# Optimization experiments

Hardware: AMD Instinct MI355X
Metric: run time of the kernel (lower is better)

Reference implementation:

```python
import jax, jax.numpy as jnp
import numpy as np

N_USER = 100000
N_ITEM = 100000
N_EDGE = 1600000
IN_U = 128
IN_I = 128
OUT = 64
NEG_SLOPE = 0.01  # torch F.leaky_relu default


def setup_inputs() -> dict:
    key = jax.random.key(0)
    ks = jax.random.split(key, 12)
    return {
        'feat_user': jax.random.normal(ks[0], (N_USER, IN_U), jnp.float32),
        'feat_item': jax.random.normal(ks[1], (N_ITEM, IN_I), jnp.float32),
        'W_user': jax.random.normal(ks[2], (IN_U, OUT), jnp.float32) * 0.05,
        'b_user': jax.random.normal(ks[3], (OUT,), jnp.float32) * 0.05,
        'W_item': jax.random.normal(ks[4], (IN_I, OUT), jnp.float32) * 0.05,
        'b_item': jax.random.normal(ks[5], (OUT,), jnp.float32) * 0.05,
        'attn_w': jax.random.normal(ks[6], (2 * OUT, 1), jnp.float32) * 0.05,
        'src_u2i': jax.random.randint(ks[7], (N_EDGE,), 0, N_USER),
        'dst_u2i': jax.random.randint(ks[8], (N_EDGE,), 0, N_ITEM),
        'src_i2u': jax.random.randint(ks[9], (N_EDGE,), 0, N_ITEM),
        'dst_i2u': jax.random.randint(ks[10], (N_EDGE,), 0, N_USER),
    }


def _segment_softmax(e, seg, num_segments):
    # e: [E], seg: [E] destination ids -> softmax over edges sharing a dst
    m = jax.ops.segment_max(e, seg, num_segments=num_segments)
    ex = jnp.exp(e - m[seg])
    s = jax.ops.segment_sum(ex, seg, num_segments=num_segments)
    return ex / s[seg]


def _etype_aggregate(Wh_src, Wh_dst, attn_w, src, dst, n_dst):
    # gather per-edge src/dst projected features: [E, OUT]
    zs = Wh_src[src]
    zd = Wh_dst[dst]
    # attn([zs || zd]) == zs @ a_src + zd @ a_dst (split the 2*OUT weight)
    a_src, a_dst = attn_w[:OUT, 0], attn_w[OUT:, 0]
    e = zs @ a_src + zd @ a_dst  # [E]
    e = jnp.where(e > 0, e, NEG_SLOPE * e)  # leaky_relu
    alpha = _segment_softmax(e, dst, n_dst)  # [E]
    # weighted scatter-sum into destination nodes
    return jax.ops.segment_sum(alpha[:, None] * zs, dst, num_segments=n_dst)


def reference(feat_user, feat_item, W_user, b_user, W_item, b_item, attn_w,
              src_u2i, dst_u2i, src_i2u, dst_i2u):
    Wh_user = feat_user @ W_user + b_user  # fc['user'] (etype 'user': user->item)
    Wh_item = feat_item @ W_item + b_item  # fc['item'] (etype 'item': item->user)
    # etype 'user': user -> item; dst attention feature is Wh_item on item nodes
    h_item = _etype_aggregate(Wh_user, Wh_item, attn_w, src_u2i, dst_u2i, N_ITEM)
    # etype 'item': item -> user
    h_user = _etype_aggregate(Wh_item, Wh_user, attn_w, src_i2u, dst_i2u, N_USER)
    # update_nodes sums all 'self_*' per ntype; each ntype has exactly one here
    return jnp.concatenate([h_user, h_item], axis=0)  # [N_USER+N_ITEM, OUT]
```

## Files before the change

### kernel.cpp

```cpp
#include <hip/hip_runtime.h>
#include <hip/hip_bf16.h>

#define NU 100000
#define NI 100000
#define NE 1600000
#define KIN 128
#define KOUT 64

#define NCOPY 8
#define PBK 128
#define NP 782
#define CAP2 384
#define CHUNK 4096
#define SRTSZ (NCOPY * CAP2 + PBK * 7)
#define AGG_THREADS 512
#define NWAVE 8

#define LIN_ROWS 64
#define LIN_GRID 512
#define LIN_ITERS 1563

typedef short bf16x8 __attribute__((ext_vector_type(8)));
typedef float f32x4  __attribute__((ext_vector_type(4)));

__device__ __forceinline__ unsigned short f2bf(float f) {
    unsigned u = __float_as_uint(f);
    unsigned r = (u + 0x7fffu + ((u >> 16) & 1u)) >> 16;
    return (unsigned short)r;
}
__device__ __forceinline__ float bf2f(unsigned short h) {
    return __uint_as_float(((unsigned)h) << 16);
}
__device__ __forceinline__ void split_bf16(float f, unsigned short& h, unsigned short& l) {
    h = f2bf(f);
    float r = f - bf2f(h);
    l = f2bf(r);
}

__global__ __launch_bounds__(256) void linear_attn_kernel(
    const float* __restrict__ A0, const float* __restrict__ W0, const float* __restrict__ bv0,
    const float* __restrict__ A1, const float* __restrict__ W1, const float* __restrict__ bv1,
    const float* __restrict__ attn,
    unsigned short* __restrict__ Wh0, float* __restrict__ su0, float* __restrict__ sd0,
    unsigned short* __restrict__ Wh1, float* __restrict__ su1, float* __restrict__ sd1)
{
    __shared__ float Al[LIN_ROWS * 132];
    __shared__ __align__(16) unsigned short Wph[4 * 4 * 64 * 8];
    __shared__ __align__(16) unsigned short Wpl[4 * 4 * 64 * 8];

    int half = gridDim.x >> 1;
    bool second = blockIdx.x >= (unsigned)half;
    const float* A = second ? A1 : A0;
    const float* W = second ? W1 : W0;
    const float* bvec = second ? bv1 : bv0;
    unsigned short* Wh = second ? Wh1 : Wh0;
    float* s_src = second ? su1 : su0;
    float* s_dst = second ? sd1 : sd0;
    int blk = second ? (blockIdx.x - half) : blockIdx.x;

    int t = threadIdx.x;
    int l   = t & 63;
    int wv  = t >> 6;
    int ln  = l & 15;
    int grp = l >> 4;

    for (int i = 0; i < 4; i++) {
        int s = t + 256 * i;
        int sl = s & 63, nt = (s >> 6) & 3, ks = s >> 8;
        int kb = ks * 32 + (sl >> 4) * 8;
        int n  = nt * 16 + (sl & 15);
        unsigned short h8[8], l8[8];
        #pragma unroll
        for (int j = 0; j < 8; j++) {
            float w = W[(size_t)(kb + j) * KOUT + n];
            split_bf16(w, h8[j], l8[j]);
        }
        int base = ((ks * 4 + nt) * 64 + sl) * 8;
        #pragma unroll
        for (int j = 0; j < 8; j++) { Wph[base + j] = h8[j]; Wpl[base + j] = l8[j]; }
    }

    float asl[4], adl[4], bl4[4];
    #pragma unroll
    for (int nt = 0; nt < 4; nt++) {
        asl[nt] = attn[nt * 16 + ln];
        adl[nt] = attn[64 + nt * 16 + ln];
        bl4[nt] = bvec[nt * 16 + ln];
    }

    int arow = wv * 16 + ln;

    for (int c = blk; c < LIN_ITERS; c += half) {
        int rowbase = c * LIN_ROWS;
        __syncthreads();
        for (int g = t; g < LIN_ROWS * 32; g += 256) {
            int rr = g >> 5;
            int q  = g & 31;
            float4 v = {0.f, 0.f, 0.f, 0.f};
            int grow = rowbase + rr;
            if (grow < NU) v = ((const float4*)(A + (size_t)grow * 128))[q];
            *(float4*)&Al[rr * 132 + q * 4] = v;
        }
        __syncthreads();

        f32x4 acc0 = {bl4[0], bl4[0], bl4[0], bl4[0]};
        f32x4 acc1 = {bl4[1], bl4[1], bl4[1], bl4[1]};
        f32x4 acc2 = {bl4[2], bl4[2], bl4[2], bl4[2]};
        f32x4 acc3 = {bl4[3], bl4[3], bl4[3], bl4[3]};

        #pragma unroll
        for (int ks = 0; ks < 4; ks++) {
            int k0 = ks * 32 + grp * 8;
            const float* ap = &Al[arow * 132 + k0];
            float4 va = *(const float4*)ap;
            float4 vb = *(const float4*)(ap + 4);
            float av[8] = {va.x, va.y, va.z, va.w, vb.x, vb.y, vb.z, vb.w};
            bf16x8 ahi, alo;
            #pragma unroll
            for (int j = 0; j < 8; j++) {
                unsigned short h, lo2;
                split_bf16(av[j], h, lo2);
                ahi[j] = (short)h; alo[j] = (short)lo2;
            }
            #pragma unroll
            for (int nt = 0; nt < 4; nt++) {
                bf16x8 bhi = *(const bf16x8*)&Wph[((ks * 4 + nt) * 64 + l) * 8];
                bf16x8 blo = *(const bf16x8*)&Wpl[((ks * 4 + nt) * 64 + l) * 8];
                f32x4 a = (nt == 0) ? acc0 : (nt == 1) ? acc1 : (nt == 2) ? acc2 : acc3;
                a = __builtin_amdgcn_mfma_f32_16x16x32_bf16(ahi, bhi, a, 0, 0, 0);
                a = __builtin_amdgcn_mfma_f32_16x16x32_bf16(ahi, blo, a, 0, 0, 0);
                a = __builtin_amdgcn_mfma_f32_16x16x32_bf16(alo, bhi, a, 0, 0, 0);
                if (nt == 0) acc0 = a; else if (nt == 1) acc1 = a; else if (nt == 2) acc2 = a; else acc3 = a;
            }
        }

        int growbase = rowbase + wv * 16;
        f32x4 accs[4] = {acc0, acc1, acc2, acc3};
        #pragma unroll
        for (int nt = 0; nt < 4; nt++) {
            #pragma unroll
            for (int r = 0; r < 4; r++) {
                int row = growbase + grp * 4 + r;
                if (row < NU) Wh[(size_t)row * KOUT + nt * 16 + ln] = f2bf(accs[nt][r]);
            }
        }
        #pragma unroll
        for (int r = 0; r < 4; r++) {
            float p1 = accs[0][r] * asl[0] + accs[1][r] * asl[1] + accs[2][r] * asl[2] + accs[3][r] * asl[3];
            float p2 = accs[0][r] * adl[0] + accs[1][r] * adl[1] + accs[2][r] * adl[2] + accs[3][r] * adl[3];
            #pragma unroll
            for (int off = 1; off < 16; off <<= 1) {
                p1 += __shfl_xor(p1, off);
                p2 += __shfl_xor(p2, off);
            }
            int row = growbase + grp * 4 + r;
            if (ln == 0 && row < NU) { s_src[row] = p1; s_dst[row] = p2; }
        }
    }
}

__global__ __launch_bounds__(256) void scatter_kernel(
    const int* __restrict__ src_u2i, const int* __restrict__ dst_u2i,
    const int* __restrict__ src_i2u, const int* __restrict__ dst_i2u,
    int* __restrict__ cur_item, int* __restrict__ cur_user,
    int* __restrict__ ebuf_item, int* __restrict__ ebuf_user,
    int nE, int nbs)
{
    __shared__ int raw[CHUNK];
    __shared__ unsigned short bkt[CHUNK];
    __shared__ int srt_[CHUNK];
    __shared__ unsigned short sbk[CHUNK];
    __shared__ int cnt[NP];
    __shared__ int gb[NP];
    __shared__ int pb[NP];
    __shared__ int lc[NP];

    bool u2i = blockIdx.x < (unsigned)nbs;
    int blk = u2i ? blockIdx.x : (blockIdx.x - nbs);
    int copy = blockIdx.x & (NCOPY - 1);
    const int* src = u2i ? src_u2i : src_i2u;
    const int* dst = u2i ? dst_u2i : dst_i2u;
    int* cur  = (u2i ? cur_item : cur_user) + copy * NP;
    int* ebuf = (u2i ? ebuf_item : ebuf_user) + (size_t)copy * NP * CAP2;

    int t = threadIdx.x;
    for (int i = t; i < NP; i += 256) cnt[i] = 0;
    __syncthreads();

    int e0 = blk * CHUNK;
    int n = nE - e0; if (n > CHUNK) n = CHUNK;

    for (int j = t; j < n; j += 256) {
        int s = src[e0 + j], d = dst[e0 + j];
        int b = d >> 7;
        raw[j] = s | ((d & 127) << 17);
        bkt[j] = (unsigned short)b;
        atomicAdd(&cnt[b], 1);
    }
    __syncthreads();

    for (int b = t; b < NP; b += 256) {
        int c = cnt[b];
        gb[b] = c ? atomicAdd(&cur[b], c) : 0;
    }
    if (t < 64) {
        int lo = t * 13;
        int hi = lo + 13; if (hi > NP) hi = NP; if (lo > NP) lo = NP;
        int s = 0;
        for (int i = lo; i < hi; i++) s += cnt[i];
        int run = s;
        #pragma unroll
        for (int off = 1; off < 64; off <<= 1) {
            int v = __shfl_up(run, off);
            if (t >= off) run += v;
        }
        int excl = run - s;
        for (int i = lo; i < hi; i++) {
            pb[i] = excl; lc[i] = excl;
            excl += cnt[i];
        }
    }
    __syncthreads();

    for (int j = t; j < n; j += 256) {
        int b = bkt[j];
        int p = atomicAdd(&lc[b], 1);
        srt_[p] = raw[j];
        sbk[p] = (unsigned short)b;
    }
    __syncthreads();

    for (int j = t; j < n; j += 256) {
        int b = sbk[j];
        int pos = gb[b] + (j - pb[b]);
        if (pos < CAP2) ebuf[(size_t)b * CAP2 + pos] = srt_[j];
    }
}

__global__ __launch_bounds__(AGG_THREADS) void agg_kernel(
    const int* __restrict__ cur_item, const int* __restrict__ cur_user,
    const int* __restrict__ ebuf_item, const int* __restrict__ ebuf_user,
    const float* __restrict__ su_user, const float* __restrict__ sd_item,
    const float* __restrict__ su_item, const float* __restrict__ sd_user,
    const unsigned short* __restrict__ Wh_user, const unsigned short* __restrict__ Wh_item,
    float* __restrict__ h_item, float* __restrict__ h_user)
{
    __shared__ int   raw[SRTSZ];
    __shared__ int   srt[SRTSZ];
    __shared__ int   offs[NCOPY + 1];
    __shared__ int   cnt[PBK];
    __shared__ int   base[PBK + 1];
    __shared__ int   cursor[PBK];
    __shared__ float sdl[PBK];

    int bid = blockIdx.x;
    bool item_side = bid < NP;
    int b = item_side ? bid : bid - NP;
    const int*   cur  = item_side ? cur_item : cur_user;
    const int*   ebuf = item_side ? ebuf_item : ebuf_user;
    const float* ssrc = item_side ? su_user : su_item;
    const float* sdst = item_side ? sd_item : sd_user;
    const unsigned short* Whs = item_side ? Wh_user : Wh_item;
    float* h = item_side ? h_item : h_user;

    int t = threadIdx.x;
    if (t < PBK) {
        cnt[t] = 0;
        int node = b * PBK + t;
        sdl[t] = (node < NU) ? sdst[node] : 0.f;
    }
    if (t == 0) {
        int a = 0;
        #pragma unroll
        for (int c = 0; c < NCOPY; c++) {
            offs[c] = a;
            int cc = cur[c * NP + b];
            if (cc > CAP2) cc = CAP2;
            a += cc;
        }
        offs[NCOPY] = a;
    }
    for (int j = t; j < SRTSZ; j += AGG_THREADS) srt[j] = 0;
    __syncthreads();

    int total = offs[NCOPY];

    for (int j = t; j < total; j += AGG_THREADS) {
        int c = 0;
        while (j >= offs[c + 1]) c++;
        int e = ebuf[((size_t)c * NP + b) * CAP2 + (j - offs[c])];
        raw[j] = e;
        atomicAdd(&cnt[e >> 17], 1);
    }
    __syncthreads();

    if (t == 0) {
        int a = 0;
        for (int i = 0; i < PBK; i++) {
            base[i] = a; cursor[i] = a;
            a += (cnt[i] + 7) & ~7;
        }
        base[PBK] = a;
    }
    __syncthreads();

    for (int j = t; j < total; j += AGG_THREADS) {
        int e = raw[j];
        int p = atomicAdd(&cursor[e >> 17], 1);
        srt[p] = e;
    }
    __syncthreads();

    int lane = t & 63;
    int wv = t >> 6;

    float* wgt = (float*)raw;
    for (int dl = wv; dl < PBK; dl += NWAVE) {
        int jb = base[dl], cc = cnt[dl], pc = base[dl + 1] - jb;
        float sd = sdl[dl];
        for (int k = lane; k < pc; k += 64) {
            float w = 0.f;
            if (k < cc) {
                int s = srt[jb + k] & 0x1FFFF;
                float ev = ssrc[s] + sd;
                ev = ev > 0.f ? ev : 0.01f * ev;
                w = __expf(ev);
            }
            wgt[jb + k] = w;
        }
    }
    __syncthreads();

    int sub = lane >> 4;
    int ch4 = (lane & 15) << 2;
    const unsigned short* WhCh = Whs + ch4;
    for (int dl = wv; dl < PBK; dl += NWAVE) {
        int node = b * PBK + dl;
        if (node >= NU) break;
        int jb = base[dl];
        int pc = base[dl + 1] - jb;
        int cc = cnt[dl];
        float ax = 0.f, ay = 0.f, az = 0.f, aw = 0.f, ssum = 0.f;
        for (int q = 0; q < pc; q += 8) {
            int j0 = jb + q + sub;
            int j1 = j0 + 4;
            int e0 = srt[j0];
            int e1 = srt[j1];
            float w0 = wgt[j0];
            float w1 = wgt[j1];
            uint2 u0 = *(const uint2*)(WhCh + ((size_t)(e0 & 0x1FFFF) << 6));
            uint2 u1 = *(const uint2*)(WhCh + ((size_t)(e1 & 0x1FFFF) << 6));
            ax += w0 * __uint_as_float(u0.x << 16)        + w1 * __uint_as_float(u1.x << 16);
            ay += w0 * __uint_as_float(u0.x & 0xffff0000u)+ w1 * __uint_as_float(u1.x & 0xffff0000u);
            az += w0 * __uint_as_float(u0.y << 16)        + w1 * __uint_as_float(u1.y << 16);
            aw += w0 * __uint_as_float(u0.y & 0xffff0000u)+ w1 * __uint_as_float(u1.y & 0xffff0000u);
            ssum += w0 + w1;
        }
        #pragma unroll
        for (int off = 16; off <= 32; off <<= 1) {
            ax += __shfl_xor(ax, off);
            ay += __shfl_xor(ay, off);
            az += __shfl_xor(az, off);
            aw += __shfl_xor(aw, off);
            ssum += __shfl_xor(ssum, off);
        }
        if (sub == 0) {
            float inv = (cc > 0) ? 1.f / ssum : 0.f;
            float4 o = {ax * inv, ay * inv, az * inv, aw * inv};
            *(float4*)(h + (size_t)node * KOUT + ch4) = o;
        }
    }
}

extern "C" void kernel_launch(void* const* d_in, const int* in_sizes, int n_in,
                              void* d_out, int out_size, void* d_ws, size_t ws_size,
                              hipStream_t stream)
{
    const float* feat_user = (const float*)d_in[0];
    const float* feat_item = (const float*)d_in[1];
    const float* W_user    = (const float*)d_in[2];
    const float* b_user    = (const float*)d_in[3];
    const float* W_item    = (const float*)d_in[4];
    const float* b_item    = (const float*)d_in[5];
    const float* attn_w    = (const float*)d_in[6];
    const int*   src_u2i   = (const int*)d_in[7];
    const int*   dst_u2i   = (const int*)d_in[8];
    const int*   src_i2u   = (const int*)d_in[9];
    const int*   dst_i2u   = (const int*)d_in[10];

    float* out    = (float*)d_out;
    float* h_user = out;
    float* h_item = out + (size_t)NU * KOUT;

    char* p = (char*)d_ws;
    unsigned short* Wh_user = (unsigned short*)p; p += (size_t)NU * KOUT * 2;
    unsigned short* Wh_item = (unsigned short*)p; p += (size_t)NI * KOUT * 2;
    float* su_user = (float*)p; p += NU * 4;
    float* sd_user = (float*)p; p += NU * 4;
    float* su_item = (float*)p; p += NI * 4;
    float* sd_item = (float*)p; p += NI * 4;
    int* cur_item  = (int*)p; p += (size_t)NCOPY * NP * 4;
    int* cur_user  = (int*)p; p += (size_t)NCOPY * NP * 4;
    int* ebuf_item = (int*)p; p += (size_t)NCOPY * NP * CAP2 * 4;
    int* ebuf_user = (int*)p; p += (size_t)NCOPY * NP * CAP2 * 4;

    hipMemsetAsync(cur_item, 0, (size_t)2 * NCOPY * NP * 4, stream);

    int nbs = (NE + CHUNK - 1) / CHUNK;
    scatter_kernel<<<2 * nbs, 256, 0, stream>>>(src_u2i, dst_u2i, src_i2u, dst_i2u,
                                                cur_item, cur_user, ebuf_item, ebuf_user,
                                                NE, nbs);
    linear_attn_kernel<<<LIN_GRID, 256, 0, stream>>>(feat_user, W_user, b_user,
                                                     feat_item, W_item, b_item, attn_w,
                                                     Wh_user, su_user, sd_user,
                                                     Wh_item, su_item, sd_item);
    agg_kernel<<<2 * NP, AGG_THREADS, 0, stream>>>(cur_item, cur_user, ebuf_item, ebuf_user,
                                                   su_user, sd_item, su_item, sd_user,
                                                   Wh_user, Wh_item, h_item, h_user);
}
```

Measured before the change: 317.9 us.

## Merge scatter and linear kernels into one interleaved launch; widen agg gathers

The edge-bucketing scatter kernel and the MFMA linear/attention kernel become one launch, with block IDs interleaved so memory-bound scatter blocks and compute-bound GEMM blocks can share the GPU at the same time and one launch boundary disappears. The agg kernel replaces a serial single-thread prefix over 128 buckets with a wave-level shuffle scan. Its gather now reads 16-byte vectors of 8 bf16 channels per lane, with 8 lanes per row and 16 edges per step, plus a tail step. The merged kernel uses a 65KB shared buffer sized for the larger role, which may lower occupancy for scatter blocks.

```diff
diff --git a/kernel.cpp b/kernel.cpp
--- a/kernel.cpp
+++ b/kernel.cpp
@@ -36,204 +36,211 @@
     float r = f - bf2f(h);
     l = f2bf(r);
 }
-
-__global__ __launch_bounds__(256) void linear_attn_kernel(
+__device__ __forceinline__ float blo(unsigned u) { return __uint_as_float(u << 16); }
+__device__ __forceinline__ float bhi(unsigned u) { return __uint_as_float(u & 0xffff0000u); }
+
+__global__ __launch_bounds__(256) void prep_kernel(
+    const int* __restrict__ src_u2i, const int* __restrict__ dst_u2i,
+    const int* __restrict__ src_i2u, const int* __restrict__ dst_i2u,
+    int* __restrict__ cur_item, int* __restrict__ cur_user,
+    int* __restrict__ ebuf_item, int* __restrict__ ebuf_user, int nE, int nbs,
     const float* __restrict__ A0, const float* __restrict__ W0, const float* __restrict__ bv0,
     const float* __restrict__ A1, const float* __restrict__ W1, const float* __restrict__ bv1,
     const float* __restrict__ attn,
     unsigned short* __restrict__ Wh0, float* __restrict__ su0, float* __restrict__ sd0,
     unsigned short* __restrict__ Wh1, float* __restrict__ su1, float* __restrict__ sd1)
 {
-    __shared__ float Al[LIN_ROWS * 132];
-    __shared__ __align__(16) unsigned short Wph[4 * 4 * 64 * 8];
-    __shared__ __align__(16) unsigned short Wpl[4 * 4 * 64 * 8];
-
-    int half = gridDim.x >> 1;
-    bool second = blockIdx.x >= (unsigned)half;
-    const float* A = second ? A1 : A0;
-    const float* W = second ? W1 : W0;
-    const float* bvec = second ? bv1 : bv0;
-    unsigned short* Wh = second ? Wh1 : Wh0;
-    float* s_src = second ? su1 : su0;
-    float* s_dst = second ? sd1 : sd0;
-    int blk = second ? (blockIdx.x - half) : blockIdx.x;
+    __shared__ __align__(16) char smem[66560];
+
+    int bid = blockIdx.x;
+    int nsc = 2 * nbs;
+    int ninter = (nsc < LIN_GRID ? nsc : LIN_GRID) * 2;
+    bool is_lin; int sid;
+    if (bid < ninter) { is_lin = (bid & 1); sid = bid >> 1; }
+    else { is_lin = false; sid = ninter / 2 + (bid - ninter); }
 
     int t = threadIdx.x;
-    int l   = t & 63;
-    int wv  = t >> 6;
-    int ln  = l & 15;
-    int grp = l >> 4;
-
-    for (int i = 0; i < 4; i++) {
-        int s = t + 256 * i;
-        int sl = s & 63, nt = (s >> 6) & 3, ks = s >> 8;
-        int kb = ks * 32 + (sl >> 4) * 8;
-        int n  = nt * 16 + (sl & 15);
-        unsigned short h8[8], l8[8];
-        #pragma unroll
-        for (int j = 0; j < 8; j++) {
-            float w = W[(size_t)(kb + j) * KOUT + n];
-            split_bf16(w, h8[j], l8[j]);
-        }
-        int base = ((ks * 4 + nt) * 64 + sl) * 8;
-        #pragma unroll
-        for (int j = 0; j < 8; j++) { Wph[base + j] = h8[j]; Wpl[base + j] = l8[j]; }
-    }
-
-    float asl[4], adl[4], bl4[4];
-    #pragma unroll
-    for (int nt = 0; nt < 4; nt++) {
-        asl[nt] = attn[nt * 16 + ln];
-        adl[nt] = attn[64 + nt * 16 + ln];
-        bl4[nt] = bvec[nt * 16 + ln];
-    }
-
-    int arow = wv * 16 + ln;
-
-    for (int c = blk; c < LIN_ITERS; c += half) {
-        int rowbase = c * LIN_ROWS;
+
+    if (!is_lin) {
+        int* raw  = (int*)smem;
+        unsigned short* bkt = (unsigned short*)(smem + 16384);
+        int* srt_ = (int*)(smem + 24576);
+        unsigned short* sbk = (unsigned short*)(smem + 40960);
+        int* cnt = (int*)(smem + 49152);
+        int* gb  = (int*)(smem + 49152 + 4 * NP);
+        int* pb  = (int*)(smem + 49152 + 8 * NP);
+        int* lc  = (int*)(smem + 49152 + 12 * NP);
+
+        bool u2i = sid < nbs;
+        int blk = u2i ? sid : (sid - nbs);
+        int copy = sid & (NCOPY - 1);
+        const int* src = u2i ? src_u2i : src_i2u;
+        const int* dst = u2i ? dst_u2i : dst_i2u;
+        int* cur  = (u2i ? cur_item : cur_user) + copy * NP;
+        int* ebuf = (u2i ? ebuf_item : ebuf_user) + (size_t)copy * NP * CAP2;
+
+        for (int i = t; i < NP; i += 256) cnt[i] = 0;
         __syncthreads();
-        for (int g = t; g < LIN_ROWS * 32; g += 256) {
-            int rr = g >> 5;
-            int q  = g & 31;
-            float4 v = {0.f, 0.f, 0.f, 0.f};
-            int grow = rowbase + rr;
-            if (grow < NU) v = ((const float4*)(A + (size_t)grow * 128))[q];
-            *(float4*)&Al[rr * 132 + q * 4] = v;
+
+        int e0 = blk * CHUNK;
+        int n = nE - e0; if (n > CHUNK) n = CHUNK;
+
+        for (int j = t; j < n; j += 256) {
+            int s = src[e0 + j], d = dst[e0 + j];
+            int b = d >> 7;
+            raw[j] = s | ((d & 127) << 17);
+            bkt[j] = (unsigned short)b;
+            atomicAdd(&cnt[b], 1);
         }
         __syncthreads();
 
-        f32x4 acc0 = {bl4[0], bl4[0], bl4[0], bl4[0]};
-        f32x4 acc1 = {bl4[1], bl4[1], bl4[1], bl4[1]};
-        f32x4 acc2 = {bl4[2], bl4[2], bl4[2], bl4[2]};
-        f32x4 acc3 = {bl4[3], bl4[3], bl4[3], bl4[3]};
-
-        #pragma unroll
-        for (int ks = 0; ks < 4; ks++) {
-            int k0 = ks * 32 + grp * 8;
-            const float* ap = &Al[arow * 132 + k0];
-            float4 va = *(const float4*)ap;
-            float4 vb = *(const float4*)(ap + 4);
-            float av[8] = {va.x, va.y, va.z, va.w, vb.x, vb.y, vb.z, vb.w};
-            bf16x8 ahi, alo;
+        for (int b = t; b < NP; b += 256) {
+            int c = cnt[b];
+            gb[b] = c ? atomicAdd(&cur[b], c) : 0;
+        }
+        if (t < 64) {
+            int lo = t * 13;
+            int hi = lo + 13; if (hi > NP) hi = NP; if (lo > NP) lo = NP;
+            int s = 0;
+            for (int i = lo; i < hi; i++) s += cnt[i];
+            int run = s;
+            #pragma unroll
+            for (int off = 1; off < 64; off <<= 1) {
+                int v = __shfl_up(run, off);
+                if (t >= off) run += v;
+            }
+            int excl = run - s;
+            for (int i = lo; i < hi; i++) {
+                pb[i] = excl; lc[i] = excl;
+                excl += cnt[i];
+            }
+        }
+        __syncthreads();
+
+        for (int j = t; j < n; j += 256) {
+            int b = bkt[j];
+            int p = atomicAdd(&lc[b], 1);
+            srt_[p] = raw[j];
+            sbk[p] = (unsigned short)b;
+        }
+        __syncthreads();
+
+        for (int j = t; j < n; j += 256) {
+            int b = sbk[j];
+            int pos = gb[b] + (j - pb[b]);
+            if (pos < CAP2) ebuf[(size_t)b * CAP2 + pos] = srt_[j];
+        }
+    } else {
+        float* Al = (float*)smem;
+        unsigned short* Wph = (unsigned short*)(smem + 33792);
+        unsigned short* Wpl = (unsigned short*)(smem + 50176);
+
+        int half = LIN_GRID / 2;
+        bool second = sid >= half;
+        const float* A = second ? A1 : A0;
+        const float* W = second ? W1 : W0;
+        const float* bvec = second ? bv1 : bv0;
+        unsigned short* Wh = second ? Wh1 : Wh0;
+        float* s_src = second ? su1 : su0;
+        float* s_dst = second ? sd1 : sd0;
+        int blk = second ? (sid - half) : sid;
+
+        int l   = t & 63;
+        int wv  = t >> 6;
+        int ln  = l & 15;
+        int grp = l >> 4;
+
+        for (int i = 0; i < 4; i++) {
+            int s = t + 256 * i;
+            int sl = s & 63, nt = (s >> 6) & 3, ks = s >> 8;
+            int kb = ks * 32 + (sl >> 4) * 8;
+            int nn = nt * 16 + (sl & 15);
+            int base = ((ks * 4 + nt) * 64 + sl) * 8;
             #pragma unroll
             for (int j = 0; j < 8; j++) {
                 unsigned short h, lo2;
-                split_bf16(av[j], h, lo2);
-                ahi[j] = (short)h; alo[j] = (short)lo2;
-            }
-            #pragma unroll
-            for (int nt = 0; nt < 4; nt++) {
-                bf16x8 bhi = *(const bf16x8*)&Wph[((ks * 4 + nt) * 64 + l) * 8];
-                bf16x8 blo = *(const bf16x8*)&Wpl[((ks * 4 + nt) * 64 + l) * 8];
-                f32x4 a = (nt == 0) ? acc0 : (nt == 1) ? acc1 : (nt == 2) ? acc2 : acc3;
-                a = __builtin_amdgcn_mfma_f32_16x16x32_bf16(ahi, bhi, a, 0, 0, 0);
-                a = __builtin_amdgcn_mfma_f32_16x16x32_bf16(ahi, blo, a, 0, 0, 0);
-                a = __builtin_amdgcn_mfma_f32_16x16x32_bf16(alo, bhi, a, 0, 0, 0);
-                if (nt == 0) acc0 = a; else if (nt == 1) acc1 = a; else if (nt == 2) acc2 = a; else acc3 = a;
-            }
-        }
-
-        int growbase = rowbase + wv * 16;
-        f32x4 accs[4] = {acc0, acc1, acc2, acc3};
+                split_bf16(W[(size_t)(kb + j) * KOUT + nn], h, lo2);
+                Wph[base + j] = h; Wpl[base + j] = lo2;
+            }
+        }
+
+        float asl[4], adl[4], bl4[4];
         #pragma unroll
         for (int nt = 0; nt < 4; nt++) {
+            asl[nt] = attn[nt * 16 + ln];
+            adl[nt] = attn[64 + nt * 16 + ln];
+            bl4[nt] = bvec[nt * 16 + ln];
+        }
+
+        int arow = wv * 16 + ln;
+
+        for (int c = blk; c < LIN_ITERS; c += half) {
+            int rowbase = c * LIN_ROWS;
+            __syncthreads();
+            for (int g = t; g < LIN_ROWS * 32; g += 256) {
+                int rr = g >> 5;
+                int q  = g & 31;
+                float4 v = {0.f, 0.f, 0.f, 0.f};
+                int grow = rowbase + rr;
+                if (grow < NU) v = ((const float4*)(A + (size_t)grow * 128))[q];
+                *(float4*)&Al[rr * 132 + q * 4] = v;
+            }
+            __syncthreads();
+
+            f32x4 acc0 = {bl4[0], bl4[0], bl4[0], bl4[0]};
+            f32x4 acc1 = {bl4[1], bl4[1], bl4[1], bl4[1]};
+            f32x4 acc2 = {bl4[2], bl4[2], bl4[2], bl4[2]};
+            f32x4 acc3 = {bl4[3], bl4[3], bl4[3], bl4[3]};
+
+            #pragma unroll
+            for (int ks = 0; ks < 4; ks++) {
+                int k0 = ks * 32 + grp * 8;
+                const float* ap = &Al[arow * 132 + k0];
+                float4 va = *(const float4*)ap;
+                float4 vb = *(const float4*)(ap + 4);
+                float av[8] = {va.x, va.y, va.z, va.w, vb.x, vb.y, vb.z, vb.w};
+                bf16x8 ahi, alo;
+                #pragma unroll
+                for (int j = 0; j < 8; j++) {
+                    unsigned short h, lo2;
+                    split_bf16(av[j], h, lo2);
+                    ahi[j] = (short)h; alo[j] = (short)lo2;
+                }
+                #pragma unroll
+                for (int nt = 0; nt < 4; nt++) {
+                    bf16x8 bhi8 = *(const bf16x8*)&Wph[((ks * 4 + nt) * 64 + l) * 8];
+                    bf16x8 blo8 = *(const bf16x8*)&Wpl[((ks * 4 + nt) * 64 + l) * 8];
+                    f32x4 a = (nt == 0) ? acc0 : (nt == 1) ? acc1 : (nt == 2) ? acc2 : acc3;
+                    a = __builtin_amdgcn_mfma_f32_16x16x32_bf16(ahi, bhi8, a, 0, 0, 0);
+                    a = __builtin_amdgcn_mfma_f32_16x16x32_bf16(ahi, blo8, a, 0, 0, 0);
+                    a = __builtin_amdgcn_mfma_f32_16x16x32_bf16(alo, bhi8, a, 0, 0, 0);
+                    if (nt == 0) acc0 = a; else if (nt == 1) acc1 = a; else if (nt == 2) acc2 = a; else acc3 = a;
+                }
+            }
+
+            int growbase = rowbase + wv * 16;
+            f32x4 accs[4] = {acc0, acc1, acc2, acc3};
+            #pragma unroll
+            for (int nt = 0; nt < 4; nt++) {
+                #pragma unroll
+                for (int r = 0; r < 4; r++) {
+                    int row = growbase + grp * 4 + r;
+                    if (row < NU) Wh[(size_t)row * KOUT + nt * 16 + ln] = f2bf(accs[nt][r]);
+                }
+            }
             #pragma unroll
             for (int r = 0; r < 4; r++) {
+                float p1 = accs[0][r] * asl[0] + accs[1][r] * asl[1] + accs[2][r] * asl[2] + accs[3][r] * asl[3];
+                float p2 = accs[0][r] * adl[0] + accs[1][r] * adl[1] + accs[2][r] * adl[2] + accs[3][r] * adl[3];
+                #pragma unroll
+                for (int off = 1; off < 16; off <<= 1) {
+                    p1 += __shfl_xor(p1, off);
+                    p2 += __shfl_xor(p2, off);
+                }
                 int row = growbase + grp * 4 + r;
-                if (row < NU) Wh[(size_t)row * KOUT + nt * 16 + ln] = f2bf(accs[nt][r]);
-            }
-        }
-        #pragma unroll
-        for (int r = 0; r < 4; r++) {
-            float p1 = accs[0][r] * asl[0] + accs[1][r] * asl[1] + accs[2][r] * asl[2] + accs[3][r] * asl[3];
-            float p2 = accs[0][r] * adl[0] + accs[1][r] * adl[1] + accs[2][r] * adl[2] + accs[3][r] * adl[3];
-            #pragma unroll
-            for (int off = 1; off < 16; off <<= 1) {
-                p1 += __shfl_xor(p1, off);
-                p2 += __shfl_xor(p2, off);
-            }
-            int row = growbase + grp * 4 + r;
-            if (ln == 0 && row < NU) { s_src[row] = p1; s_dst[row] = p2; }
-        }
-    }
-}
-
-__global__ __launch_bounds__(256) void scatter_kernel(
-    const int* __restrict__ src_u2i, const int* __restrict__ dst_u2i,
-    const int* __restrict__ src_i2u, const int* __restrict__ dst_i2u,
-    int* __restrict__ cur_item, int* __restrict__ cur_user,
-    int* __restrict__ ebuf_item, int* __restrict__ ebuf_user,
-    int nE, int nbs)
-{
-    __shared__ int raw[CHUNK];
-    __shared__ unsigned short bkt[CHUNK];
-    __shared__ int srt_[CHUNK];
-    __shared__ unsigned short sbk[CHUNK];
-    __shared__ int cnt[NP];
-    __shared__ int gb[NP];
-    __shared__ int pb[NP];
-    __shared__ int lc[NP];
-
-    bool u2i = blockIdx.x < (unsigned)nbs;
-    int blk = u2i ? blockIdx.x : (blockIdx.x - nbs);
-    int copy = blockIdx.x & (NCOPY - 1);
-    const int* src = u2i ? src_u2i : src_i2u;
-    const int* dst = u2i ? dst_u2i : dst_i2u;
-    int* cur  = (u2i ? cur_item : cur_user) + copy * NP;
-    int* ebuf = (u2i ? ebuf_item : ebuf_user) + (size_t)copy * NP * CAP2;
-
-    int t = threadIdx.x;
-    for (int i = t; i < NP; i += 256) cnt[i] = 0;
-    __syncthreads();
-
-    int e0 = blk * CHUNK;
-    int n = nE - e0; if (n > CHUNK) n = CHUNK;
-
-    for (int j = t; j < n; j += 256) {
-        int s = src[e0 + j], d = dst[e0 + j];
-        int b = d >> 7;
-        raw[j] = s | ((d & 127) << 17);
-        bkt[j] = (unsigned short)b;
-        atomicAdd(&cnt[b], 1);
-    }
-    __syncthreads();
-
-    for (int b = t; b < NP; b += 256) {
-        int c = cnt[b];
-        gb[b] = c ? atomicAdd(&cur[b], c) : 0;
-    }
-    if (t < 64) {
-        int lo = t * 13;
-        int hi = lo + 13; if (hi > NP) hi = NP; if (lo > NP) lo = NP;
-        int s = 0;
-        for (int i = lo; i < hi; i++) s += cnt[i];
-        int run = s;
-        #pragma unroll
-        for (int off = 1; off < 64; off <<= 1) {
-            int v = __shfl_up(run, off);
-            if (t >= off) run += v;
-        }
-        int excl = run - s;
-        for (int i = lo; i < hi; i++) {
-            pb[i] = excl; lc[i] = excl;
-            excl += cnt[i];
-        }
-    }
-    __syncthreads();
-
-    for (int j = t; j < n; j += 256) {
-        int b = bkt[j];
-        int p = atomicAdd(&lc[b], 1);
-        srt_[p] = raw[j];
-        sbk[p] = (unsigned short)b;
-    }
-    __syncthreads();
-
-    for (int j = t; j < n; j += 256) {
-        int b = sbk[j];
-        int pos = gb[b] + (j - pb[b]);
-        if (pos < CAP2) ebuf[(size_t)b * CAP2 + pos] = srt_[j];
+                if (ln == 0 && row < NU) { s_src[row] = p1; s_dst[row] = p2; }
+            }
+        }
     }
 }
 
@@ -294,13 +301,21 @@
     }
     __syncthreads();
 
-    if (t == 0) {
-        int a = 0;
-        for (int i = 0; i < PBK; i++) {
-            base[i] = a; cursor[i] = a;
-            a += (cnt[i] + 7) & ~7;
-        }
-        base[PBK] = a;
+    if (t < 64) {
+        int i0 = 2 * t, i1 = 2 * t + 1;
+        int c0 = (cnt[i0] + 7) & ~7;
+        int c1 = (cnt[i1] + 7) & ~7;
+        int s = c0 + c1;
+        int run = s;
+        #pragma unroll
+        for (int off = 1; off < 64; off <<= 1) {
+            int v = __shfl_up(run, off);
+            if (t >= off) run += v;
+        }
+        int excl = run - s;
+        base[i0] = excl;      cursor[i0] = excl;
+        base[i1] = excl + c0; cursor[i1] = excl + c0;
+        if (t == 63) base[PBK] = run;
     }
     __syncthreads();
 
@@ -331,43 +346,60 @@
     }
     __syncthreads();
 
-    int sub = lane >> 4;
-    int ch4 = (lane & 15) << 2;
-    const unsigned short* WhCh = Whs + ch4;
+    int sub = lane >> 3;
+    int ch8 = (lane & 7) << 3;
+    const unsigned short* WhCh = Whs + ch8;
     for (int dl = wv; dl < PBK; dl += NWAVE) {
         int node = b * PBK + dl;
         if (node >= NU) break;
         int jb = base[dl];
         int pc = base[dl + 1] - jb;
         int cc = cnt[dl];
-        float ax = 0.f, ay = 0.f, az = 0.f, aw = 0.f, ssum = 0.f;
-        for (int q = 0; q < pc; q += 8) {
+        float acc[8] = {0.f, 0.f, 0.f, 0.f, 0.f, 0.f, 0.f, 0.f};
+        float ssum = 0.f;
+        int q = 0;
+        for (; q + 16 <= pc; q += 16) {
             int j0 = jb + q + sub;
-            int j1 = j0 + 4;
-            int e0 = srt[j0];
-            int e1 = srt[j1];
-            float w0 = wgt[j0];
-            float w1 = wgt[j1];
-            uint2 u0 = *(const uint2*)(WhCh + ((size_t)(e0 & 0x1FFFF) << 6));
-            uint2 u1 = *(const uint2*)(WhCh + ((size_t)(e1 & 0x1FFFF) << 6));
-            ax += w0 * __uint_as_float(u0.x << 16)        + w1 * __uint_as_float(u1.x << 16);
-            ay += w0 * __uint_as_float(u0.x & 0xffff0000u)+ w1 * __uint_as_float(u1.x & 0xffff0000u);
-            az += w0 * __uint_as_float(u0.y << 16)        + w1 * __uint_as_float(u1.y << 16);
-            aw += w0 * __uint_as_float(u0.y & 0xffff0000u)+ w1 * __uint_as_float(u1.y & 0xffff0000u);
+            int j1 = j0 + 8;
+            int e0 = srt[j0], e1 = srt[j1];
+            float w0 = wgt[j0], w1 = wgt[j1];
+            uint4 u0 = *(const uint4*)(WhCh + ((size_t)(e0 & 0x1FFFF) << 6));
+            uint4 u1 = *(const uint4*)(WhCh + ((size_t)(e1 & 0x1FFFF) << 6));
+            unsigned a4[4] = {u0.x, u0.y, u0.z, u0.w};
+            unsigned b4[4] = {u1.x, u1.y, u1.z, u1.w};
+            #pragma unroll
+            for (int ii = 0; ii < 4; ii++) {
+                acc[2 * ii]     += w0 * blo(a4[ii]) + w1 * blo(b4[ii]);
+                acc[2 * ii + 1] += w0 * bhi(a4[ii]) + w1 * bhi(b4[ii]);
+            }
             ssum += w0 + w1;
         }
+        if (q < pc) {
+            int j = jb + q + sub;
+            int e = srt[j];
+            float w = wgt[j];
+            uint4 u = *(const uint4*)(WhCh + ((size_t)(e & 0x1FFFF) << 6));
+            unsigned a4[4] = {u.x, u.y, u.z, u.w};
+            #pragma unroll
+            for (int ii = 0; ii < 4; ii++) {
+                acc[2 * ii]     += w * blo(a4[ii]);
+                acc[2 * ii + 1] += w * bhi(a4[ii]);
+            }
+            ssum += w;
+        }
         #pragma unroll
-        for (int off = 16; off <= 32; off <<= 1) {
-            ax += __shfl_xor(ax, off);
-            ay += __shfl_xor(ay, off);
-            az += __shfl_xor(az, off);
-            aw += __shfl_xor(aw, off);
+        for (int off = 8; off <= 32; off <<= 1) {
+            #pragma unroll
+            for (int ii = 0; ii < 8; ii++) acc[ii] += __shfl_xor(acc[ii], off);
             ssum += __shfl_xor(ssum, off);
         }
         if (sub == 0) {
             float inv = (cc > 0) ? 1.f / ssum : 0.f;
-            float4 o = {ax * inv, ay * inv, az * inv, aw * inv};
-            *(float4*)(h + (size_t)node * KOUT + ch4) = o;
+            float4 o0 = {acc[0] * inv, acc[1] * inv, acc[2] * inv, acc[3] * inv};
+            float4 o1 = {acc[4] * inv, acc[5] * inv, acc[6] * inv, acc[7] * inv};
+            float* hp = h + (size_t)node * KOUT + ch8;
+            *(float4*)hp = o0;
+            *(float4*)(hp + 4) = o1;
         }
     }
 }
@@ -407,13 +439,13 @@
     hipMemsetAsync(cur_item, 0, (size_t)2 * NCOPY * NP * 4, stream);
 
     int nbs = (NE + CHUNK - 1) / CHUNK;
-    scatter_kernel<<<2 * nbs, 256, 0, stream>>>(src_u2i, dst_u2i, src_i2u, dst_i2u,
-                                                cur_item, cur_user, ebuf_item, ebuf_user,
-                                                NE, nbs);
-    linear_attn_kernel<<<LIN_GRID, 256, 0, stream>>>(feat_user, W_user, b_user,
-                                                     feat_item, W_item, b_item, attn_w,
-                                                     Wh_user, su_user, sd_user,
-                                                     Wh_item, su_item, sd_item);
+    int grid = 2 * nbs + LIN_GRID;
+    prep_kernel<<<grid, 256, 0, stream>>>(src_u2i, dst_u2i, src_i2u, dst_i2u,
+                                          cur_item, cur_user, ebuf_item, ebuf_user, NE, nbs,
+                                          feat_user, W_user, b_user,
+                                          feat_item, W_item, b_item, attn_w,
+                                          Wh_user, su_user, sd_user,
+                                          Wh_item, su_item, sd_item);
     agg_kernel<<<2 * NP, AGG_THREADS, 0, stream>>>(cur_item, cur_user, ebuf_item, ebuf_user,
                                                    su_user, sd_item, su_item, sd_user,
                                                    Wh_user, Wh_item, h_item, h_user);
```

New measurement: 351.1 us. 1.1x slower.
